# Performance work log

Measured on AMD Instinct MI355X. Metric: run time of the kernel, lower is better.

The kernel has to match this reference:

```python
import jax, jax.numpy as jnp
import numpy as np

B, S, H = 2, 1024, 2048
D = 256          # index_dimension = min(index.embedding_dimension, hidden_size)
R = 32           # LoRA rank
K = 4            # index_k neighbors per query token
N_DB = 100000    # rows in the external index


def setup_inputs() -> dict:
    key = jax.random.key(0)
    ks = jax.random.split(key, 7)
    return {
        "hidden_states": jax.random.normal(ks[0], (B, S, H), jnp.float32),
        "db_keys": jax.random.normal(ks[1], (N_DB, D), jnp.float32),
        "db_values": jax.random.normal(ks[2], (N_DB, D), jnp.float32),
        "wq_in": jax.random.normal(ks[3], (H, R), jnp.float32) * 0.02,
        "wq_out": jax.random.normal(ks[4], (R, D), jnp.float32) * 0.02,
        "wv_in": jax.random.normal(ks[5], (D, R), jnp.float32) * 0.02,
        "wv_out": jax.random.normal(ks[6], (R, H), jnp.float32) * 0.02,
    }


def reference(hidden_states, db_keys, db_values, wq_in, wq_out, wv_in, wv_out):
    b, s, h = hidden_states.shape
    d = wq_out.shape[1]
    # query LoRA projection: hidden -> r -> index_dim
    q = (hidden_states @ wq_in) @ wq_out            # [B, S, D]

    # external k-NN lookup (exact L2 top-k over index table), no_grad in torch
    qf = q.reshape(b * s, d)                        # [B*S, D]
    qn = jnp.sum(qf * qf, axis=-1, keepdims=True)   # [B*S, 1]
    kn = jnp.sum(db_keys * db_keys, axis=-1)        # [N_DB]
    dist = qn - 2.0 * (qf @ db_keys.T) + kn[None, :]  # [B*S, N_DB]
    _, idx = jax.lax.top_k(-dist, K)                # [B*S, K] nearest neighbors

    # gather KV and reshape to [B, S*K, D] (matches torch view calls)
    kv_key = jax.lax.stop_gradient(db_keys[idx]).reshape(b, s * K, d)
    kv_val = jax.lax.stop_gradient(db_values[idx]).reshape(b, s * K, d)

    # SDPA, is_causal=True with Lq != Lk: top-left aligned tril mask (j <= i)
    scale = 1.0 / np.sqrt(d).astype(np.float32)
    scores = jnp.einsum('bqd,bkd->bqk', q, kv_key) * scale  # [B, S, S*K]
    mask = jnp.arange(s * K)[None, :] <= jnp.arange(s)[:, None]
    scores = jnp.where(mask[None, :, :], scores, jnp.finfo(scores.dtype).min)
    attn = jax.nn.softmax(scores, axis=-1)
    out = jnp.einsum('bqk,bkd->bqd', attn, kv_val)  # [B, S, D]

    # value LoRA projection: index_dim -> r -> hidden
    return (out @ wv_in) @ wv_out                   # [B, S, H]
```

## Files before the change

kernel.cpp:

```cpp
#include <hip/hip_runtime.h>
#include <cfloat>

#define B_   2
#define S_   1024
#define H_   2048
#define D_   256
#define R_   32
#define K_   4
#define NDB_ 100000

#define TSEL 256
#define NSEL (B_ * TSEL)

#define NCHUNK     61
#define CHUNK_ROWS 1664
#define TILES      13
#define NT         128
#define MT         64
#define KC         64
#define LSTR       68

#define NEG_INF  (-3.0e38f)
#define IDX_MAX  0x7fffffff

#define OFF_Q     0
#define OFF_KN    0x200000
#define OFF_PS    0x280000
#define OFF_PI    0x300000
#define OFF_IDX   0x380000
#define OFF_CAND  0x3A0000
#define OFF_KVT   0x400000
#define OFF_AO    0x600000
#define OFF_DBK16 0x800000

typedef unsigned short ushort_t;
typedef unsigned int   uint_t;
typedef __attribute__((ext_vector_type(8)))  __bf16 bf16x8;
typedef __attribute__((ext_vector_type(16))) float  f32x16;

__device__ __forceinline__ void ins4(float sc, int n, float s[4], int id[4]) {
  if (sc > s[3] || (sc == s[3] && n < id[3])) {
    s[3] = sc; id[3] = n;
#pragma unroll
    for (int k = 3; k > 0; --k) {
      if (s[k] > s[k - 1] || (s[k] == s[k - 1] && id[k] < id[k - 1])) {
        float ts = s[k]; s[k] = s[k - 1]; s[k - 1] = ts;
        int ti = id[k]; id[k] = id[k - 1]; id[k - 1] = ti;
      }
    }
  }
}

__device__ __forceinline__ uint_t bfpack(float a, float b) {
  uint_t ua = __float_as_uint(a), ub = __float_as_uint(b);
  ua = (ua + 0x7fffu + ((ua >> 16) & 1u)) >> 16;
  ub = (ub + 0x7fffu + ((ub >> 16) & 1u)) >> 16;
  return ua | (ub << 16);
}

__global__ __launch_bounds__(256) void k_compute_q(
    const float* __restrict__ hidden, const float* __restrict__ wq_in,
    const float* __restrict__ wq_out, float* __restrict__ q) {
  __shared__ float hrow[H_];
  __shared__ float part[8][R_];
  __shared__ float q1[R_];
  const int m = blockIdx.x;
  const int t = threadIdx.x;
  const float* hp = hidden + (size_t)m * H_;
  ((float4*)hrow)[t]       = ((const float4*)hp)[t];
  ((float4*)hrow)[t + 256] = ((const float4*)hp)[t + 256];
  __syncthreads();
  const int r = t & 31, c = t >> 5;
  float p = 0.f;
#pragma unroll 4
  for (int e = c * 256; e < c * 256 + 256; ++e)
    p = fmaf(hrow[e], wq_in[(size_t)e * R_ + r], p);
  part[c][r] = p;
  __syncthreads();
  if (t < R_) {
    float s = 0.f;
#pragma unroll
    for (int cc = 0; cc < 8; ++cc) s += part[cc][t];
    q1[t] = s;
  }
  __syncthreads();
  float acc = 0.f;
#pragma unroll
  for (int rr = 0; rr < R_; ++rr) acc = fmaf(q1[rr], wq_out[rr * D_ + t], acc);
  q[(size_t)m * D_ + t] = acc;
}

__global__ __launch_bounds__(256) void k_kn_cvt(const float* __restrict__ dbk,
                                               float* __restrict__ kn,
                                               ushort_t* __restrict__ dbk16) {
  const int w = threadIdx.x >> 6, l = threadIdx.x & 63;
  const int n = blockIdx.x * 4 + w;
  if (n >= NDB_) return;
  const float4 v = ((const float4*)(dbk + (size_t)n * D_))[l];
  uint2 p; p.x = bfpack(v.x, v.y); p.y = bfpack(v.z, v.w);
  ((uint2*)(dbk16 + (size_t)n * D_))[l] = p;
  float s = v.x * v.x + v.y * v.y + v.z * v.z + v.w * v.w;
#pragma unroll
  for (int off = 32; off; off >>= 1) s += __shfl_down(s, off);
  if (l == 0) kn[n] = s;
}

__global__ __launch_bounds__(256) void k_kn(const float* __restrict__ dbk,
                                            float* __restrict__ kn) {
  const int w = threadIdx.x >> 6, l = threadIdx.x & 63;
  const int n = blockIdx.x * 4 + w;
  if (n >= NDB_) return;
  const float4 v = ((const float4*)(dbk + (size_t)n * D_))[l];
  float s = v.x * v.x + v.y * v.y + v.z * v.z + v.w * v.w;
#pragma unroll
  for (int off = 32; off; off >>= 1) s += __shfl_down(s, off);
  if (l == 0) kn[n] = s;
}

__global__ __launch_bounds__(256, 2) void k_knn_mfma(
    const float* __restrict__ q, const ushort_t* __restrict__ dbk16,
    const float* __restrict__ kn, float* __restrict__ pscore,
    int* __restrict__ pidx) {
  __shared__ __align__(16) char smem[65536];
  ushort_t* sA = (ushort_t*)smem;
  ushort_t* sB = (ushort_t*)(smem + 32768);
  float*    sS = (float*)(smem + 32768);

  const int tid = threadIdx.x;
  const int wv = tid >> 6, ln = tid & 63;
  const int lm = ln & 31, lh = ln >> 5;
  const int tx = tid & 15, ty = tid >> 4;
  const int chunk = blockIdx.x, qb = blockIdx.y;
  const int row_base = chunk * CHUNK_ROWS;

  {
    const int m = tid & 63, cg = tid >> 6;
    const int sq = qb * MT + m;
    const float* qp = q + ((size_t)((sq >> 8) * S_ + (sq & 255))) * D_;
#pragma unroll
    for (int cc = 0; cc < 8; ++cc) {
      const int c = cg * 8 + cc;
      const float4 v0 = *(const float4*)(qp + c * 8);
      const float4 v1 = *(const float4*)(qp + c * 8 + 4);
      uint4 pk;
      pk.x = bfpack(v0.x, v0.y); pk.y = bfpack(v0.z, v0.w);
      pk.z = bfpack(v1.x, v1.y); pk.w = bfpack(v1.z, v1.w);
      *(uint4*)&sA[(m * 32 + (c ^ (m & 7))) * 8] = pk;
    }
  }

  float s4[4][4]; int i4[4][4];
#pragma unroll
  for (int a = 0; a < 4; ++a)
#pragma unroll
    for (int b = 0; b < 4; ++b) { s4[a][b] = NEG_INF; i4[a][b] = IDX_MAX; }

  for (int tile = 0; tile < TILES; ++tile) {
    const int row0 = row_base + tile * NT;
    if (row0 >= NDB_) break;

    f32x16 acc0, acc1;
#pragma unroll
    for (int r = 0; r < 16; ++r) { acc0[r] = 0.f; acc1[r] = 0.f; }

    for (int kh = 0; kh < 2; ++kh) {
      __syncthreads();
      {
        const int n_in = ln >> 4;
        const int p    = ln & 15;
#pragma unroll
        for (int i = 0; i < 8; ++i) {
          const int nloc = wv * 32 + i * 4 + n_in;
          int krow = row0 + nloc; if (krow >= NDB_) krow = NDB_ - 1;
          const int c = p ^ (nloc & 7);
          const ushort_t* gp = dbk16 + (size_t)krow * D_ + (kh * 16 + c) * 8;
          ushort_t* lp = sB + (size_t)(wv * 32 + i * 4) * 128;
          __builtin_amdgcn_global_load_lds(
              (const __attribute__((address_space(1))) void*)gp,
              (__attribute__((address_space(3))) void*)lp, 16, 0, 0);
        }
      }
      __syncthreads();
      const int nB = wv * 32 + lm;
      const int bswz = nB & 7;
#pragma unroll
      for (int ks = 0; ks < 8; ++ks) {
        const int cA = kh * 16 + ks * 2 + lh;
        const bf16x8 a0 = *(const bf16x8*)&sA[(lm * 32 + (cA ^ (lm & 7))) * 8];
        const bf16x8 a1 = *(const bf16x8*)&sA[((32 + lm) * 32 + (cA ^ (lm & 7))) * 8];
        const bf16x8 bb = *(const bf16x8*)&sB[(nB * 16 + ((ks * 2 + lh) ^ bswz)) * 8];
        acc0 = __builtin_amdgcn_mfma_f32_32x32x16_bf16(a0, bb, acc0, 0, 0, 0);
        acc1 = __builtin_amdgcn_mfma_f32_32x32x16_bf16(a1, bb, acc1, 0, 0, 0);
      }
    }
    __syncthreads();
    {
      const int n = wv * 32 + lm;
#pragma unroll
      for (int r = 0; r < 16; ++r) {
        const int mrow = (r & 3) + 8 * (r >> 2) + 4 * lh;
        sS[mrow * 128 + n]        = acc0[r];
        sS[(32 + mrow) * 128 + n] = acc1[r];
      }
    }
    __syncthreads();
    {
      float knv[8]; int nok[8];
#pragma unroll
      for (int j = 0; j < 8; ++j) {
        const int n = row0 + tx * 8 + j;
        nok[j] = (n < NDB_);
        knv[j] = nok[j] ? kn[n] : 0.f;
      }
#pragma unroll
      for (int qi = 0; qi < 4; ++qi) {
        const int m = ty * 4 + qi;
        const float4 v0 = *(const float4*)&sS[m * 128 + tx * 8];
        const float4 v1 = *(const float4*)&sS[m * 128 + tx * 8 + 4];
        const float sv[8] = {v0.x, v0.y, v0.z, v0.w, v1.x, v1.y, v1.z, v1.w};
#pragma unroll
        for (int j = 0; j < 8; ++j)
          if (nok[j]) ins4(2.f * sv[j] - knv[j], row0 + tx * 8 + j, s4[qi], i4[qi]);
      }
    }
  }

  __syncthreads();
  float* cs = (float*)smem;
  int*   ci = (int*)(smem + 64 * 65 * 4);
#pragma unroll
  for (int qi = 0; qi < 4; ++qi)
#pragma unroll
    for (int k = 0; k < 4; ++k) {
      cs[(ty * 4 + qi) * 65 + tx * 4 + k] = s4[qi][k];
      ci[(ty * 4 + qi) * 65 + tx * 4 + k] = i4[qi][k];
    }
  __syncthreads();
  if (tid < 64) {
    float fs[4]; int fi[4];
#pragma unroll
    for (int k = 0; k < 4; ++k) { fs[k] = NEG_INF; fi[k] = IDX_MAX; }
    for (int c = 0; c < 64; ++c)
      ins4(cs[tid * 65 + c], ci[tid * 65 + c], fs, fi);
    const int sq = qb * MT + tid;
    float* po = pscore + ((size_t)sq * NCHUNK + chunk) * 4;
    int*   io = pidx   + ((size_t)sq * NCHUNK + chunk) * 4;
#pragma unroll
    for (int k = 0; k < 4; ++k) { po[k] = fs[k]; io[k] = fi[k]; }
  }
}

__global__ __launch_bounds__(256) void k_knn_partial(
    const float* __restrict__ q, const float* __restrict__ dbk,
    const float* __restrict__ kn, float* __restrict__ pscore,
    int* __restrict__ pidx) {
  __shared__ float smem[3 * KC * LSTR];
  float* sA  = smem;
  float* sB0 = smem + KC * LSTR;
  float* sB1 = smem + 2 * KC * LSTR;
  const int tid = threadIdx.x;
  const int tx = tid & 15, ty = tid >> 4;
  const int chunk = blockIdx.x, qb = blockIdx.y;
  const int arq = tid >> 2;
  const int aqd = (tid & 3) * 4;
  const int brk = tid >> 1;
  const int bh  = tid & 1;
  const int bcol = ((brk >> 3) << 2) | (brk & 3);
  float* sBw = (brk & 4) ? sB1 : sB0;
  const int sq_a = qb * MT + arq;
  const float* qsrc = q + ((size_t)((sq_a >> 8) * S_ + (sq_a & 255))) * D_;
  float s4[4][4]; int i4[4][4];
#pragma unroll
  for (int a = 0; a < 4; ++a)
#pragma unroll
    for (int b = 0; b < 4; ++b) { s4[a][b] = NEG_INF; i4[a][b] = IDX_MAX; }
  const int row_base = chunk * CHUNK_ROWS;
  for (int tile = 0; tile < TILES; ++tile) {
    const int row0 = row_base + tile * NT;
    if (row0 >= NDB_) break;
    int krow = row0 + brk; if (krow >= NDB_) krow = NDB_ - 1;
    const float* ksrc = dbk + (size_t)krow * D_;
    float acc[4][8];
#pragma unroll
    for (int a = 0; a < 4; ++a)
#pragma unroll
      for (int b = 0; b < 8; ++b) acc[a][b] = 0.f;
    for (int kc = 0; kc < 4; ++kc) {
      __syncthreads();
#pragma unroll
      for (int p = 0; p < 4; ++p) {
        const int kkl = p * 16 + aqd;
        const float4 v = *(const float4*)(qsrc + kc * KC + kkl);
        sA[(kkl + 0) * LSTR + arq] = v.x;
        sA[(kkl + 1) * LSTR + arq] = v.y;
        sA[(kkl + 2) * LSTR + arq] = v.z;
        sA[(kkl + 3) * LSTR + arq] = v.w;
      }
#pragma unroll
      for (int p = 0; p < 8; ++p) {
        const int kkl = bh * 32 + p * 4;
        const float4 v = *(const float4*)(ksrc + kc * KC + kkl);
        sBw[(kkl + 0) * LSTR + bcol] = v.x;
        sBw[(kkl + 1) * LSTR + bcol] = v.y;
        sBw[(kkl + 2) * LSTR + bcol] = v.z;
        sBw[(kkl + 3) * LSTR + bcol] = v.w;
      }
      __syncthreads();
#pragma unroll 4
      for (int kk = 0; kk < KC; ++kk) {
        const float4 a  = *(const float4*)&sA [kk * LSTR + ty * 4];
        const float4 b0 = *(const float4*)&sB0[kk * LSTR + tx * 4];
        const float4 b1 = *(const float4*)&sB1[kk * LSTR + tx * 4];
        const float av[4] = {a.x, a.y, a.z, a.w};
        const float bv[8] = {b0.x, b0.y, b0.z, b0.w, b1.x, b1.y, b1.z, b1.w};
#pragma unroll
        for (int qi = 0; qi < 4; ++qi)
#pragma unroll
          for (int nj = 0; nj < 8; ++nj)
            acc[qi][nj] = fmaf(av[qi], bv[nj], acc[qi][nj]);
      }
    }
#pragma unroll
    for (int nj = 0; nj < 8; ++nj) {
      const int n = row0 + tx * 8 + nj;
      if (n < NDB_) {
        const float knj = kn[n];
        ins4(2.f * acc[0][nj] - knj, n, s4[0], i4[0]);
        ins4(2.f * acc[1][nj] - knj, n, s4[1], i4[1]);
        ins4(2.f * acc[2][nj] - knj, n, s4[2], i4[2]);
        ins4(2.f * acc[3][nj] - knj, n, s4[3], i4[3]);
      }
    }
  }
  __syncthreads();
  float* cs = smem;
  int*   ci = (int*)(smem + 64 * 65);
#pragma unroll
  for (int qi = 0; qi < 4; ++qi)
#pragma unroll
    for (int k = 0; k < 4; ++k) {
      cs[(ty * 4 + qi) * 65 + tx * 4 + k] = s4[qi][k];
      ci[(ty * 4 + qi) * 65 + tx * 4 + k] = i4[qi][k];
    }
  __syncthreads();
  if (tid < 64) {
    float fs[4]; int fi[4];
#pragma unroll
    for (int k = 0; k < 4; ++k) { fs[k] = NEG_INF; fi[k] = IDX_MAX; }
    for (int c = 0; c < 64; ++c)
      ins4(cs[tid * 65 + c], ci[tid * 65 + c], fs, fi);
    const int sq = qb * MT + tid;
    float* po = pscore + ((size_t)sq * NCHUNK + chunk) * 4;
    int*   io = pidx   + ((size_t)sq * NCHUNK + chunk) * 4;
#pragma unroll
    for (int k = 0; k < 4; ++k) { po[k] = fs[k]; io[k] = fi[k]; }
  }
}

template <int RANKS>
__device__ __forceinline__ void merge_top(const float* __restrict__ pscore,
                                          const int* __restrict__ pidx,
                                          int* __restrict__ outp) {
  const int sq = blockIdx.x, l = threadIdx.x;
  float s4[4]; int i4[4];
#pragma unroll
  for (int k = 0; k < 4; ++k) { s4[k] = NEG_INF; i4[k] = IDX_MAX; }
  for (int c = l; c < NCHUNK * 4; c += 64)
    ins4(pscore[(size_t)sq * NCHUNK * 4 + c], pidx[(size_t)sq * NCHUNK * 4 + c], s4, i4);
#pragma unroll
  for (int r = 0; r < RANKS; ++r) {
    float s = s4[0]; int i = i4[0];
#pragma unroll
    for (int off = 32; off; off >>= 1) {
      float so = __shfl_down(s, off); int io = __shfl_down(i, off);
      if (so > s || (so == s && io < i)) { s = so; i = io; }
    }
    const float sw = __shfl(s, 0); const int iw = __shfl(i, 0);
    if (l == 0) outp[sq * RANKS + r] = iw;
    if (s4[0] == sw && i4[0] == iw) {
      s4[0] = s4[1]; i4[0] = i4[1];
      s4[1] = s4[2]; i4[1] = i4[2];
      s4[2] = s4[3]; i4[2] = i4[3];
      s4[3] = NEG_INF; i4[3] = IDX_MAX;
    }
  }
}

__global__ __launch_bounds__(64) void k_knn_merge4(const float* __restrict__ ps,
                                                   const int* __restrict__ pi,
                                                   int* __restrict__ knn_idx) {
  merge_top<4>(ps, pi, knn_idx);
}
__global__ __launch_bounds__(64) void k_knn_merge16(const float* __restrict__ ps,
                                                    const int* __restrict__ pi,
                                                    int* __restrict__ cand) {
  merge_top<16>(ps, pi, cand);
}

__global__ __launch_bounds__(256) void k_rescore(const float* __restrict__ q,
                                                 const float* __restrict__ dbk,
                                                 const float* __restrict__ kn,
                                                 const int* __restrict__ cand,
                                                 int* __restrict__ knn_idx) {
  __shared__ float scs[16];
  __shared__ int   sci[16];
  const int sq = blockIdx.x, wv = threadIdx.x >> 6, l = threadIdx.x & 63;
  const float* qp = q + ((size_t)((sq >> 8) * S_ + (sq & 255))) * D_;
  const float4 qv = ((const float4*)qp)[l];
  for (int cc = wv; cc < 16; cc += 4) {
    const int n = cand[sq * 16 + cc];
    const float4 kv = ((const float4*)(dbk + (size_t)n * D_))[l];
    float s = qv.x * kv.x + qv.y * kv.y + qv.z * kv.z + qv.w * kv.w;
#pragma unroll
    for (int off = 32; off; off >>= 1) s += __shfl_down(s, off);
    if (l == 0) { scs[cc] = 2.f * s - kn[n]; sci[cc] = n; }
  }
  __syncthreads();
  if (threadIdx.x == 0) {
    float s4[4]; int i4[4];
#pragma unroll
    for (int k = 0; k < 4; ++k) { s4[k] = NEG_INF; i4[k] = IDX_MAX; }
#pragma unroll
    for (int c = 0; c < 16; ++c) ins4(scs[c], sci[c], s4, i4);
#pragma unroll
    for (int k = 0; k < 4; ++k) knn_idx[sq * 4 + k] = i4[k];
  }
}

__global__ __launch_bounds__(256) void k_gather(const float* __restrict__ dbk,
                                                const int* __restrict__ knn_idx,
                                                float* __restrict__ kvT) {
  const int b = blockIdx.x >> 6, j0 = (blockIdx.x & 63) * 16;
  const int w = threadIdx.x >> 6, l = threadIdx.x & 63;
  float* dst = kvT + (size_t)b * D_ * 1024;
  for (int jj = w; jj < 16; jj += 4) {
    const int j = j0 + jj;
    const int row = knn_idx[b * 1024 + j];
    const float4 v = ((const float4*)(dbk + (size_t)row * D_))[l];
    dst[(4 * l + 0) * 1024 + j] = v.x;
    dst[(4 * l + 1) * 1024 + j] = v.y;
    dst[(4 * l + 2) * 1024 + j] = v.z;
    dst[(4 * l + 3) * 1024 + j] = v.w;
  }
}

__global__ __launch_bounds__(256) void k_attn(const float* __restrict__ qarr,
                                              const float* __restrict__ kvT,
                                              const int* __restrict__ knn_idx,
                                              const float* __restrict__ dbv,
                                              float* __restrict__ attout) {
  __shared__ float qrow[D_];
  __shared__ float attw[1024];
  __shared__ int   jrow[1024];
  __shared__ float red1[4], red2[4];
  const int b = blockIdx.x >> 10, i = blockIdx.x & 1023;
  const int t = threadIdx.x;
  const int nk = i + 1;
  qrow[t] = qarr[((size_t)b * S_ + i) * D_ + t];
  for (int j = t; j < 1024; j += 256) jrow[j] = knn_idx[b * 1024 + j];
  __syncthreads();
  const int cmax = (nk + 255) >> 8;
  const float scale = 0.0625f;
  float sc[4]; float mloc = NEG_INF;
#pragma unroll
  for (int c = 0; c < 4; ++c) {
    sc[c] = NEG_INF;
    if (c < cmax) {
      const int j = c * 256 + t;
      float a = 0.f;
      const float* kp = kvT + (size_t)b * D_ * 1024 + j;
#pragma unroll 8
      for (int d = 0; d < D_; ++d) a = fmaf(qrow[d], kp[(size_t)d * 1024], a);
      if (j < nk) sc[c] = a * scale;
    }
    mloc = fmaxf(mloc, sc[c]);
  }
#pragma unroll
  for (int off = 32; off; off >>= 1) mloc = fmaxf(mloc, __shfl_down(mloc, off));
  if ((t & 63) == 0) red1[t >> 6] = mloc;
  __syncthreads();
  const float mmax = fmaxf(fmaxf(red1[0], red1[1]), fmaxf(red1[2], red1[3]));
  float sloc = 0.f; float pv[4];
#pragma unroll
  for (int c = 0; c < 4; ++c) {
    pv[c] = (sc[c] > NEG_INF * 0.5f) ? __expf(sc[c] - mmax) : 0.f;
    sloc += pv[c];
  }
#pragma unroll
  for (int off = 32; off; off >>= 1) sloc += __shfl_down(sloc, off);
  if ((t & 63) == 0) red2[t >> 6] = sloc;
  __syncthreads();
  const float inv = 1.f / (red2[0] + red2[1] + red2[2] + red2[3]);
#pragma unroll
  for (int c = 0; c < 4; ++c)
    if (c < cmax) attw[c * 256 + t] = pv[c] * inv;
  __syncthreads();
  float a0 = 0.f, a1 = 0.f, a2 = 0.f, a3 = 0.f;
  int j = 0;
  for (; j + 4 <= nk; j += 4) {
    a0 = fmaf(attw[j + 0], dbv[(size_t)jrow[j + 0] * D_ + t], a0);
    a1 = fmaf(attw[j + 1], dbv[(size_t)jrow[j + 1] * D_ + t], a1);
    a2 = fmaf(attw[j + 2], dbv[(size_t)jrow[j + 2] * D_ + t], a2);
    a3 = fmaf(attw[j + 3], dbv[(size_t)jrow[j + 3] * D_ + t], a3);
  }
  for (; j < nk; ++j) a0 = fmaf(attw[j], dbv[(size_t)jrow[j] * D_ + t], a0);
  attout[((size_t)b * S_ + i) * D_ + t] = (a0 + a1) + (a2 + a3);
}

__global__ __launch_bounds__(256) void k_out(const float* __restrict__ attout,
                                             const float* __restrict__ wv_in,
                                             const float* __restrict__ wv_out,
                                             float* __restrict__ y) {
  __shared__ float row[D_];
  __shared__ float part[8][R_];
  __shared__ float t32[R_];
  const int m = blockIdx.x, t = threadIdx.x;
  row[t] = attout[(size_t)m * D_ + t];
  __syncthreads();
  const int r = t & 31, c = t >> 5;
  float p = 0.f;
#pragma unroll
  for (int d = c * 32; d < c * 32 + 32; ++d)
    p = fmaf(row[d], wv_in[d * R_ + r], p);
  part[c][r] = p;
  __syncthreads();
  if (t < R_) {
    float s = 0.f;
#pragma unroll
    for (int cc = 0; cc < 8; ++cc) s += part[cc][t];
    t32[t] = s;
  }
  __syncthreads();
  for (int hh = t; hh < H_; hh += 256) {
    float a = 0.f;
#pragma unroll
    for (int rr = 0; rr < R_; ++rr) a = fmaf(t32[rr], wv_out[rr * H_ + hh], a);
    y[(size_t)m * H_ + hh] = a;
  }
}

extern "C" void kernel_launch(void* const* d_in, const int* in_sizes, int n_in,
                              void* d_out, int out_size, void* d_ws, size_t ws_size,
                              hipStream_t stream) {
  const float* hidden  = (const float*)d_in[0];
  const float* db_keys = (const float*)d_in[1];
  const float* db_vals = (const float*)d_in[2];
  const float* wq_in   = (const float*)d_in[3];
  const float* wq_out  = (const float*)d_in[4];
  const float* wv_in   = (const float*)d_in[5];
  const float* wv_out  = (const float*)d_in[6];
  float* out = (float*)d_out;

  char* ws = (char*)d_ws;
  float*    q      = (float*)(ws + OFF_Q);
  float*    kn     = (float*)(ws + OFF_KN);
  float*    ps     = (float*)(ws + OFF_PS);
  int*      pi     = (int*)  (ws + OFF_PI);
  int*      idx    = (int*)  (ws + OFF_IDX);
  int*      cand   = (int*)  (ws + OFF_CAND);
  float*    kvT    = (float*)(ws + OFF_KVT);
  float*    attout = (float*)(ws + OFF_AO);
  ushort_t* dbk16  = (ushort_t*)(ws + OFF_DBK16);

  const size_t need = (size_t)OFF_DBK16 + (size_t)NDB_ * D_ * 2;

  k_compute_q<<<B_ * S_, 256, 0, stream>>>(hidden, wq_in, wq_out, q);
  if (ws_size >= need) {
    k_kn_cvt<<<(NDB_ + 3) / 4, 256, 0, stream>>>(db_keys, kn, dbk16);
    k_knn_mfma<<<dim3(NCHUNK, 8), 256, 0, stream>>>(q, dbk16, kn, ps, pi);
    k_knn_merge16<<<NSEL, 64, 0, stream>>>(ps, pi, cand);
    k_rescore<<<NSEL, 256, 0, stream>>>(q, db_keys, kn, cand, idx);
  } else {
    k_kn<<<(NDB_ + 3) / 4, 256, 0, stream>>>(db_keys, kn);
    k_knn_partial<<<dim3(NCHUNK, 8), 256, 0, stream>>>(q, db_keys, kn, ps, pi);
    k_knn_merge4<<<NSEL, 64, 0, stream>>>(ps, pi, idx);
  }
  k_gather<<<2 * 64, 256, 0, stream>>>(db_keys, idx, kvT);
  k_attn<<<B_ * S_, 256, 0, stream>>>(q, kvT, idx, db_vals, attout);
  k_out<<<B_ * S_, 256, 0, stream>>>(attout, wv_in, wv_out, out);
}
```

Baseline: 550.6 us.

## Pre-gather value rows contiguously, reorder kNN grid, add early-out top-4 filter

The gather kernel now also copies the selected value rows into a contiguous per-batch buffer. The attention kernel reads that buffer directly instead of doing indirect dbv lookups through a shared index array. The kNN MFMA grid is transposed so the 8 query blocks sharing a chunk of database rows launch next to each other, which should improve L2 reuse of the bf16 keys. The top-4 insertion now computes the max of each 8-score group and skips the insert loop when no score can enter the list. The cost is an extra 2 MB workspace region, a shifted dbk16 offset, and an extra write pass in the gather.

Result: no change. 544.4 us (-1.1%).

```diff
diff --git a/kernel.cpp b/kernel.cpp
--- a/kernel.cpp
+++ b/kernel.cpp
@@ -31,7 +31,8 @@
 #define OFF_CAND  0x3A0000
 #define OFF_KVT   0x400000
 #define OFF_AO    0x600000
-#define OFF_DBK16 0x800000
+#define OFF_KVV   0x800000
+#define OFF_DBK16 0xA00000
 
 typedef unsigned short ushort_t;
 typedef unsigned int   uint_t;
@@ -130,7 +131,7 @@
   const int wv = tid >> 6, ln = tid & 63;
   const int lm = ln & 31, lh = ln >> 5;
   const int tx = tid & 15, ty = tid >> 4;
-  const int chunk = blockIdx.x, qb = blockIdx.y;
+  const int qb = blockIdx.x, chunk = blockIdx.y;
   const int row_base = chunk * CHUNK_ROWS;
 
   {
@@ -194,8 +195,9 @@
       }
     }
     __syncthreads();
+
     {
-      const int n = wv * 32 + lm;
+      const int n = (tid >> 6) * 32 + lm;
 #pragma unroll
       for (int r = 0; r < 16; ++r) {
         const int mrow = (r & 3) + 8 * (r >> 2) + 4 * lh;
@@ -204,13 +206,14 @@
       }
     }
     __syncthreads();
+
     {
+      const int nbase = row0 + tx * 8;
       float knv[8]; int nok[8];
 #pragma unroll
       for (int j = 0; j < 8; ++j) {
-        const int n = row0 + tx * 8 + j;
-        nok[j] = (n < NDB_);
-        knv[j] = nok[j] ? kn[n] : 0.f;
+        nok[j] = (nbase + j < NDB_);
+        knv[j] = nok[j] ? kn[nbase + j] : 0.f;
       }
 #pragma unroll
       for (int qi = 0; qi < 4; ++qi) {
@@ -218,9 +221,17 @@
         const float4 v0 = *(const float4*)&sS[m * 128 + tx * 8];
         const float4 v1 = *(const float4*)&sS[m * 128 + tx * 8 + 4];
         const float sv[8] = {v0.x, v0.y, v0.z, v0.w, v1.x, v1.y, v1.z, v1.w};
+        float v[8];
 #pragma unroll
         for (int j = 0; j < 8; ++j)
-          if (nok[j]) ins4(2.f * sv[j] - knv[j], row0 + tx * 8 + j, s4[qi], i4[qi]);
+          v[j] = nok[j] ? fmaf(2.f, sv[j], -knv[j]) : NEG_INF;
+        const float mx = fmaxf(fmaxf(fmaxf(v[0], v[1]), fmaxf(v[2], v[3])),
+                               fmaxf(fmaxf(v[4], v[5]), fmaxf(v[6], v[7])));
+        if (mx >= s4[qi][3]) {
+#pragma unroll
+          for (int j = 0; j < 8; ++j)
+            if (nok[j]) ins4(v[j], nbase + j, s4[qi], i4[qi]);
+        }
       }
     }
   }
@@ -428,36 +439,38 @@
 }
 
 __global__ __launch_bounds__(256) void k_gather(const float* __restrict__ dbk,
+                                                const float* __restrict__ dbv,
                                                 const int* __restrict__ knn_idx,
-                                                float* __restrict__ kvT) {
+                                                float* __restrict__ kvT,
+                                                float* __restrict__ kvV) {
   const int b = blockIdx.x >> 6, j0 = (blockIdx.x & 63) * 16;
   const int w = threadIdx.x >> 6, l = threadIdx.x & 63;
-  float* dst = kvT + (size_t)b * D_ * 1024;
+  float* dstT = kvT + (size_t)b * D_ * 1024;
+  float* dstV = kvV + (size_t)b * 1024 * D_;
   for (int jj = w; jj < 16; jj += 4) {
     const int j = j0 + jj;
     const int row = knn_idx[b * 1024 + j];
-    const float4 v = ((const float4*)(dbk + (size_t)row * D_))[l];
-    dst[(4 * l + 0) * 1024 + j] = v.x;
-    dst[(4 * l + 1) * 1024 + j] = v.y;
-    dst[(4 * l + 2) * 1024 + j] = v.z;
-    dst[(4 * l + 3) * 1024 + j] = v.w;
+    const float4 kv = ((const float4*)(dbk + (size_t)row * D_))[l];
+    dstT[(4 * l + 0) * 1024 + j] = kv.x;
+    dstT[(4 * l + 1) * 1024 + j] = kv.y;
+    dstT[(4 * l + 2) * 1024 + j] = kv.z;
+    dstT[(4 * l + 3) * 1024 + j] = kv.w;
+    const float4 vv = ((const float4*)(dbv + (size_t)row * D_))[l];
+    ((float4*)(dstV + (size_t)j * D_))[l] = vv;
   }
 }
 
 __global__ __launch_bounds__(256) void k_attn(const float* __restrict__ qarr,
                                               const float* __restrict__ kvT,
-                                              const int* __restrict__ knn_idx,
-                                              const float* __restrict__ dbv,
+                                              const float* __restrict__ kvV,
                                               float* __restrict__ attout) {
   __shared__ float qrow[D_];
   __shared__ float attw[1024];
-  __shared__ int   jrow[1024];
   __shared__ float red1[4], red2[4];
   const int b = blockIdx.x >> 10, i = blockIdx.x & 1023;
   const int t = threadIdx.x;
   const int nk = i + 1;
   qrow[t] = qarr[((size_t)b * S_ + i) * D_ + t];
-  for (int j = t; j < 1024; j += 256) jrow[j] = knn_idx[b * 1024 + j];
   __syncthreads();
   const int cmax = (nk + 255) >> 8;
   const float scale = 0.0625f;
@@ -495,15 +508,16 @@
   for (int c = 0; c < 4; ++c)
     if (c < cmax) attw[c * 256 + t] = pv[c] * inv;
   __syncthreads();
+  const float* vb = kvV + (size_t)b * 1024 * D_;
   float a0 = 0.f, a1 = 0.f, a2 = 0.f, a3 = 0.f;
   int j = 0;
   for (; j + 4 <= nk; j += 4) {
-    a0 = fmaf(attw[j + 0], dbv[(size_t)jrow[j + 0] * D_ + t], a0);
-    a1 = fmaf(attw[j + 1], dbv[(size_t)jrow[j + 1] * D_ + t], a1);
-    a2 = fmaf(attw[j + 2], dbv[(size_t)jrow[j + 2] * D_ + t], a2);
-    a3 = fmaf(attw[j + 3], dbv[(size_t)jrow[j + 3] * D_ + t], a3);
-  }
-  for (; j < nk; ++j) a0 = fmaf(attw[j], dbv[(size_t)jrow[j] * D_ + t], a0);
+    a0 = fmaf(attw[j + 0], vb[(size_t)(j + 0) * D_ + t], a0);
+    a1 = fmaf(attw[j + 1], vb[(size_t)(j + 1) * D_ + t], a1);
+    a2 = fmaf(attw[j + 2], vb[(size_t)(j + 2) * D_ + t], a2);
+    a3 = fmaf(attw[j + 3], vb[(size_t)(j + 3) * D_ + t], a3);
+  }
+  for (; j < nk; ++j) a0 = fmaf(attw[j], vb[(size_t)j * D_ + t], a0);
   attout[((size_t)b * S_ + i) * D_ + t] = (a0 + a1) + (a2 + a3);
 }
 
@@ -560,6 +574,7 @@
   int*      cand   = (int*)  (ws + OFF_CAND);
   float*    kvT    = (float*)(ws + OFF_KVT);
   float*    attout = (float*)(ws + OFF_AO);
+  float*    kvV    = (float*)(ws + OFF_KVV);
   ushort_t* dbk16  = (ushort_t*)(ws + OFF_DBK16);
 
   const size_t need = (size_t)OFF_DBK16 + (size_t)NDB_ * D_ * 2;
@@ -567,7 +582,7 @@
   k_compute_q<<<B_ * S_, 256, 0, stream>>>(hidden, wq_in, wq_out, q);
   if (ws_size >= need) {
     k_kn_cvt<<<(NDB_ + 3) / 4, 256, 0, stream>>>(db_keys, kn, dbk16);
-    k_knn_mfma<<<dim3(NCHUNK, 8), 256, 0, stream>>>(q, dbk16, kn, ps, pi);
+    k_knn_mfma<<<dim3(8, NCHUNK), 256, 0, stream>>>(q, dbk16, kn, ps, pi);
     k_knn_merge16<<<NSEL, 64, 0, stream>>>(ps, pi, cand);
     k_rescore<<<NSEL, 256, 0, stream>>>(q, db_keys, kn, cand, idx);
   } else {
@@ -575,7 +590,7 @@
     k_knn_partial<<<dim3(NCHUNK, 8), 256, 0, stream>>>(q, db_keys, kn, ps, pi);
     k_knn_merge4<<<NSEL, 64, 0, stream>>>(ps, pi, idx);
   }
-  k_gather<<<2 * 64, 256, 0, stream>>>(db_keys, idx, kvT);
-  k_attn<<<B_ * S_, 256, 0, stream>>>(q, kvT, idx, db_vals, attout);
+  k_gather<<<2 * 64, 256, 0, stream>>>(db_keys, db_vals, idx, kvT, kvV);
+  k_attn<<<B_ * S_, 256, 0, stream>>>(q, kvT, kvV, attout);
   k_out<<<B_ * S_, 256, 0, stream>>>(attout, wv_in, wv_out, out);
 }
```
